# Kernel tuning notes

Hardware: AMD Instinct MI355X
Metric: run time of the kernel (lower is better)

## Reference

```python
import jax, jax.numpy as jnp
import numpy as np

B, S, D = 2, 2048, 1024
HQ, HKV = 16, 4
HD = D // HQ            # 64
RATIO = HQ // HKV       # 4
P = 4 * D               # 4096 FFN project dim
ROPE_BASE = 10000.0
NEG = -1e9


def _rope(x):
    # x: [..., s, d]; half-split (non-alternating) RoPE
    d = x.shape[-1]
    s = x.shape[-2]
    inv = 1.0 / (ROPE_BASE ** (jnp.arange(0, d, 2, dtype=jnp.float32) / d))
    ang = jnp.arange(s, dtype=jnp.float32)[:, None] * inv[None, :]   # [s, d/2]
    cos, sin = jnp.cos(ang), jnp.sin(ang)
    x1, x2 = x[..., : d // 2], x[..., d // 2 :]
    return jnp.concatenate([x1 * cos - x2 * sin, x1 * sin + x2 * cos], axis=-1)


def _layernorm(x, g, b):
    m = jnp.mean(x, axis=-1, keepdims=True)
    v = jnp.var(x, axis=-1, keepdims=True)
    return (x - m) * jax.lax.rsqrt(v + 1e-5) * g + b


def setup_inputs() -> dict:
    key = jax.random.key(0)
    ks = jax.random.split(key, 16)
    sd = 0.02
    x = jax.random.normal(ks[0], (B, S, D), dtype=jnp.float32)
    mask = jnp.where(jnp.tril(jnp.ones((S, S), dtype=bool)), 0.0, NEG).astype(jnp.float32)
    return {
        "x": x,
        "attention_mask": mask,
        "wq": jax.random.normal(ks[1], (D, D)) * sd,
        "wk": jax.random.normal(ks[2], (D, HKV * HD)) * sd,
        "wv": jax.random.normal(ks[3], (D, HKV * HD)) * sd,
        "wo": jax.random.normal(ks[4], (D, D)) * sd,
        "ln1_g": jnp.ones((D,), jnp.float32),
        "ln1_b": jnp.zeros((D,), jnp.float32),
        "ln2_g": jnp.ones((D,), jnp.float32),
        "ln2_b": jnp.zeros((D,), jnp.float32),
        "w1": jax.random.normal(ks[5], (D, P)) * sd,
        "b1": jnp.zeros((P,), jnp.float32),
        "w2": jax.random.normal(ks[6], (P, D)) * sd,
        "b2": jnp.zeros((D,), jnp.float32),
    }


def reference(x, attention_mask, wq, wk, wv, wo, ln1_g, ln1_b, ln2_g, ln2_b, w1, b1, w2, b2):
    b, s, d = x.shape
    # --- pre-norm GQA attention ---
    h = _layernorm(x, ln1_g, ln1_b)
    q = (h @ wq).reshape(b, s, HQ, HD).transpose(0, 2, 1, 3)       # [b, HQ, s, hd]
    k = (h @ wk).reshape(b, s, HKV, HD).transpose(0, 2, 1, 3)      # [b, HKV, s, hd]
    v = (h @ wv).reshape(b, s, HKV, HD).transpose(0, 2, 1, 3)
    q = _rope(q)
    k = _rope(k)
    # '(head group)' split with group = num_heads_kv, faithful to source
    q = q.reshape(b, RATIO, HKV, s, HD)                            # [b, r, g, s, hd]
    scores = jnp.einsum('brgsd,bgtd->brgst', q, k) / np.float32(np.sqrt(HD))
    scores = scores + attention_mask                               # broadcast [s,s]
    att = jax.nn.softmax(scores, axis=-1)
    o = jnp.einsum('brgst,bgtd->brgsd', att, v)                    # [b, r, g, s, hd]
    # '... head group s dhead -> ... s (head group dhead)'
    o = o.transpose(0, 3, 1, 2, 4).reshape(b, s, d)
    x = x + o @ wo
    # --- pre-norm MLP ---
    h2 = _layernorm(x, ln2_g, ln2_b)
    mlp = jax.nn.gelu(h2 @ w1 + b1) @ w2 + b2
    return x + mlp
```

## Files before the change

kernel.cpp:

```cpp
#include <hip/hip_runtime.h>
#include <cstdint>
#include <cstddef>

#define B_   2
#define S_   2048
#define D_   1024
#define HQ_  16
#define HKV_ 4
#define HD_  64
#define P_   4096

using frag8 = __attribute__((ext_vector_type(8))) short;
using f32x4 = __attribute__((ext_vector_type(4))) float;

__device__ __forceinline__ uint16_t f2b(float f) {
  uint32_t u = __builtin_bit_cast(uint32_t, f);
  u += 0x7fffu + ((u >> 16) & 1u);
  return (uint16_t)(u >> 16);
}
__device__ __forceinline__ float b2f(uint16_t h) {
  return __builtin_bit_cast(float, (uint32_t)h << 16);
}

__device__ __forceinline__ void gl16(const uint16_t* g, uint16_t* l) {
  __builtin_amdgcn_global_load_lds(
      (const __attribute__((address_space(1))) void*)g,
      (__attribute__((address_space(3))) void*)l, 16, 0, 0);
}

__device__ __forceinline__ float ldr(const void* p, size_t i, bool f32) {
  return f32 ? ((const float*)p)[i] : b2f(((const uint16_t*)p)[i]);
}
__device__ __forceinline__ void str_(void* p, size_t i, float v, bool f32) {
  if (f32) ((float*)p)[i] = v; else ((uint16_t*)p)[i] = f2b(v);
}

template <int CTRL>
__device__ __forceinline__ float fdpp(float x) {
  int v = __builtin_amdgcn_mov_dpp(__builtin_bit_cast(int, x), CTRL, 0xf, 0xf, true);
  return __builtin_bit_cast(float, v);
}
__device__ __forceinline__ float row16_max(float x) {
  x = fmaxf(x, fdpp<0xB1>(x));
  x = fmaxf(x, fdpp<0x4E>(x));
  x = fmaxf(x, fdpp<0x124>(x));
  x = fmaxf(x, fdpp<0x128>(x));
  return x;
}
__device__ __forceinline__ float row16_sum(float x) {
  x += fdpp<0xB1>(x);
  x += fdpp<0x4E>(x);
  x += fdpp<0x124>(x);
  x += fdpp<0x128>(x);
  return x;
}

__device__ __forceinline__ int psw(int row, int col) {
  return (((row) << 7) + ((col) << 1)) ^ ((row & 7) << 4);
}

__global__ void detect_kernel(const uint16_t* __restrict__ x, int* __restrict__ flag) {
  if (threadIdx.x == 0 && blockIdx.x == 0) {
    int sane = 0;
    for (int i = 0; i < 256; ++i) {
      uint16_t u = x[i];
      int e = (u >> 7) & 0xFF;
      if (u == 0 || (e >= 90 && e <= 141)) sane++;
    }
    *flag = (sane >= 240) ? 0 : 1;
  }
}

__global__ __launch_bounds__(256) void rope_table_kernel(float* __restrict__ cosT,
                                                         float* __restrict__ sinT) {
  int i = blockIdx.x * 256 + threadIdx.x;
  int s = i >> 5, d = i & 31;
  float ang = (float)s * powf(10000.0f, -(float)d * (1.0f / 32.0f));
  cosT[i] = cosf(ang);
  sinT[i] = sinf(ang);
}

template <bool F32>
__device__ __forceinline__ void trans_body(const void* in, uint16_t* out, int K, int N,
                                           uint16_t (*tile)[33]) {
  int n0 = blockIdx.x * 32, k0 = blockIdx.y * 32;
  int tx = threadIdx.x & 31, ty = threadIdx.x >> 5;
#pragma unroll
  for (int i = 0; i < 32; i += 8) {
    size_t idx = (size_t)(k0 + ty + i) * N + n0 + tx;
    tile[ty + i][tx] = F32 ? f2b(((const float*)in)[idx]) : ((const uint16_t*)in)[idx];
  }
  __syncthreads();
#pragma unroll
  for (int i = 0; i < 32; i += 8) out[(size_t)(n0 + ty + i) * K + k0 + tx] = tile[tx][ty + i];
}
__global__ __launch_bounds__(256) void transpose_k(const void* __restrict__ in,
                                                   uint16_t* __restrict__ out,
                                                   int K, int N, const int* __restrict__ flag) {
  __shared__ uint16_t tile[32][33];
  if (*flag) trans_body<true>(in, out, K, N, tile);
  else       trans_body<false>(in, out, K, N, tile);
}

template <bool F32>
__device__ __forceinline__ void ln_body(const void* x, const void* gamma, const void* beta,
                                        uint16_t* out, float* red) {
  const int row = blockIdx.x;
  const int t = threadIdx.x;
  float f[4], s1 = 0.f, s2 = 0.f;
#pragma unroll
  for (int i = 0; i < 4; i++) {
    f[i] = F32 ? ((const float*)x)[(size_t)row * D_ + t * 4 + i]
               : b2f(((const uint16_t*)x)[(size_t)row * D_ + t * 4 + i]);
    s1 += f[i]; s2 += f[i] * f[i];
  }
  for (int off = 1; off < 64; off <<= 1) { s1 += __shfl_xor(s1, off); s2 += __shfl_xor(s2, off); }
  int wave = t >> 6;
  if ((t & 63) == 0) { red[wave] = s1; red[4 + wave] = s2; }
  __syncthreads();
  s1 = red[0] + red[1] + red[2] + red[3];
  s2 = red[4] + red[5] + red[6] + red[7];
  float mean = s1 * (1.f / D_);
  float var = s2 * (1.f / D_) - mean * mean;
  float rstd = rsqrtf(var + 1e-5f);
  uint16_t ov[4];
#pragma unroll
  for (int i = 0; i < 4; i++) {
    float gv = F32 ? ((const float*)gamma)[t * 4 + i] : b2f(((const uint16_t*)gamma)[t * 4 + i]);
    float bv = F32 ? ((const float*)beta)[t * 4 + i]  : b2f(((const uint16_t*)beta)[t * 4 + i]);
    ov[i] = f2b((f[i] - mean) * rstd * gv + bv);
  }
  *(uint64_t*)(out + (size_t)row * D_ + t * 4) = *(uint64_t*)ov;
}
__global__ __launch_bounds__(256) void ln_kernel(const void* __restrict__ x,
                                                 const void* __restrict__ gamma,
                                                 const void* __restrict__ beta,
                                                 uint16_t* __restrict__ out,
                                                 const int* __restrict__ flag) {
  __shared__ float red[8];
  if (*flag) ln_body<true>(x, gamma, beta, out, red);
  else       ln_body<false>(x, gamma, beta, out, red);
}

enum { EPI_ROPE = 1, EPI_TRANSV = 2, EPI_GELU = 3, EPI_RES = 4, EPI_ACC = 5 };

template <int EPI>
__global__ __launch_bounds__(256) void gemm_bt(const uint16_t* __restrict__ A, int lda,
                                               const uint16_t* __restrict__ Bt, int ldb,
                                               void* __restrict__ C, int ldc,
                                               int M, int N, int K,
                                               const float* __restrict__ cosT,
                                               const float* __restrict__ sinT,
                                               const void* __restrict__ bias, int bias_off,
                                               const void* __restrict__ res,
                                               const int* __restrict__ flag) {
  __shared__ __align__(16) uint16_t As[2][64 * 64];
  __shared__ __align__(16) uint16_t Bs[2][64 * 64];
  const int tid = threadIdx.x;
  const int wave = tid >> 6, lane = tid & 63;
  const int quad = lane >> 4, l15 = lane & 15;
  const int bm = blockIdx.x * 64, bn = blockIdx.y * 64;
  const bool f32 = flag ? (*flag != 0) : false;

  const int arow = tid >> 3;
  const int gcol = (tid & 7) ^ (arow & 7);
  const uint16_t* apt = A + (size_t)(bm + arow) * lda + gcol * 8;
  const uint16_t* bpt = Bt + (size_t)(bn + arow) * ldb + gcol * 8;
  const int woff = wave * 512;

  f32x4 acc[4];
  f32x4 zero = {0.f, 0.f, 0.f, 0.f};
#pragma unroll
  for (int j = 0; j < 4; j++) acc[j] = zero;

  auto stage = [&](int buf, int it) {
    const uint16_t* a = apt + it * 64;
    const uint16_t* b = bpt + it * 64;
    gl16(a,                     &As[buf][woff]);
    gl16(a + (size_t)32 * lda,  &As[buf][2048 + woff]);
    gl16(b,                     &Bs[buf][woff]);
    gl16(b + (size_t)32 * ldb,  &Bs[buf][2048 + woff]);
  };

  const int NIT = K >> 6;
  stage(0, 0);
  int cur = 0;
  for (int it = 0; it < NIT; ++it) {
    stage(cur ^ 1, (it + 1 < NIT) ? (it + 1) : it);
    asm volatile("s_waitcnt vmcnt(4)" ::: "memory");
    __builtin_amdgcn_s_barrier();
    asm volatile("" ::: "memory");
    frag8 af[2], bfv[4][2];
#pragma unroll
    for (int ks = 0; ks < 2; ++ks) {
      int row = wave * 16 + l15;
      int c16 = (ks * 4 + quad) ^ (l15 & 7);
      af[ks] = *(const frag8*)&As[cur][row * 64 + c16 * 8];
    }
#pragma unroll
    for (int ni = 0; ni < 4; ++ni)
#pragma unroll
      for (int ks = 0; ks < 2; ++ks) {
        int row = ni * 16 + l15;
        int c16 = (ks * 4 + quad) ^ (l15 & 7);
        bfv[ni][ks] = *(const frag8*)&Bs[cur][row * 64 + c16 * 8];
      }
#pragma unroll
    for (int ks = 0; ks < 2; ++ks)
#pragma unroll
      for (int ni = 0; ni < 4; ++ni)
        acc[ni] = __builtin_amdgcn_mfma_f32_16x16x32_bf16(af[ks], bfv[ni][ks], acc[ni], 0, 0, 0);
    asm volatile("s_waitcnt lgkmcnt(0)" ::: "memory");
    __builtin_amdgcn_s_barrier();
    cur ^= 1;
  }

  const int row0 = bm + wave * 16 + quad * 4;

  if constexpr (EPI == EPI_ROPE) {
#pragma unroll
    for (int r = 0; r < 4; ++r) {
      int row = row0 + r;
      int s = row & (S_ - 1);
#pragma unroll
      for (int ni = 0; ni < 2; ++ni) {
        int d = ni * 16 + l15;
        float c = cosT[s * 32 + d], sn = sinT[s * 32 + d];
        float x1 = acc[ni][r], x2 = acc[ni + 2][r];
        size_t base = (size_t)row * ldc + bn + ni * 16 + l15;
        ((uint16_t*)C)[base] = f2b(x1 * c - x2 * sn);
        ((uint16_t*)C)[base + 32] = f2b(x1 * sn + x2 * c);
      }
    }
  } else if constexpr (EPI == EPI_TRANSV) {
#pragma unroll
    for (int ni = 0; ni < 4; ++ni)
#pragma unroll
      for (int r = 0; r < 4; ++r) {
        int row = row0 + r;
        int col = bn + ni * 16 + l15;
        int b = row >> 11, s = row & (S_ - 1);
        int kvh = col >> 6, d = col & 63;
        ((uint16_t*)C)[(size_t)((b * HKV_ + kvh) * HD_ + d) * S_ + s] = f2b(acc[ni][r]);
      }
  } else {
#pragma unroll
    for (int ni = 0; ni < 4; ++ni) {
      int col = bn + ni * 16 + l15;
#pragma unroll
      for (int r = 0; r < 4; ++r) {
        int row = row0 + r;
        float v = acc[ni][r];
        if constexpr (EPI == EPI_GELU) {
          v += ldr(bias, bias_off + col, f32);
          float z = 0.7978845608028654f * (v + 0.044715f * v * v * v);
          z = fminf(fmaxf(z, -15.f), 15.f);
          float e = __expf(-2.f * z);
          v = 0.5f * v * (1.f + (1.f - e) / (1.f + e));
          ((uint16_t*)C)[(size_t)row * ldc + col] = f2b(v);
        } else if constexpr (EPI == EPI_RES) {
          v += ldr(res, (size_t)row * ldc + col, f32);
          str_(C, (size_t)row * ldc + col, v, f32);
        } else if constexpr (EPI == EPI_ACC) {
          if (bias) v += ldr(bias, bias_off + col, f32);
          v += ldr(C, (size_t)row * ldc + col, f32);
          str_(C, (size_t)row * ldc + col, v, f32);
        }
      }
    }
  }
}

__global__ __launch_bounds__(256, 4) void attn_kernel(const uint16_t* __restrict__ q,
                                                      const uint16_t* __restrict__ k,
                                                      const uint16_t* __restrict__ vt,
                                                      uint16_t* __restrict__ o) {
  __shared__ __align__(16) uint16_t Ks[2][64 * 64];
  __shared__ __align__(16) uint16_t Vs[2][64 * 64];
  __shared__ __align__(16) uint16_t Plds[4][16 * 64];
  const int tid = threadIdx.x;
  const int wave = tid >> 6, lane = tid & 63;
  const int quad = lane >> 4, l15 = lane & 15;
  const int bid = blockIdx.x;
  const int m = bid & 63;
  const int g = (bid >> 6) & 3;
  const int b = bid >> 8;
  const int h = g + 4 * wave;

  const uint16_t* kbase = k + (size_t)(b * S_) * (HKV_ * HD_) + g * HD_;
  const uint16_t* vbase = vt + (size_t)((b * HKV_ + g) * HD_) * S_;
  f32x4 zero = {0.f, 0.f, 0.f, 0.f};

  const int arow = tid >> 3;
  const int gcol = (tid & 7) ^ (arow & 7);
  const int woff = wave * 512;
  uint16_t* pw = Plds[wave];

  auto stage = [&](int buf, int t) {
    const int kt = t << 6;
    gl16(kbase + (size_t)(kt + arow) * (HKV_ * HD_) + gcol * 8,      &Ks[buf][woff]);
    gl16(kbase + (size_t)(kt + 32 + arow) * (HKV_ * HD_) + gcol * 8, &Ks[buf][2048 + woff]);
    gl16(vbase + (size_t)arow * S_ + kt + gcol * 8,                  &Vs[buf][woff]);
    gl16(vbase + (size_t)(arow + 32) * S_ + kt + gcol * 8,           &Vs[buf][2048 + woff]);
  };

  int cur = 0;
  for (int seg = 0; seg < 2; ++seg) {
    const int qt = seg ? (127 - m) : m;
    const int q0 = qt * 16;

    const uint16_t* qbase = q + (size_t)(b * S_ + q0 + l15) * D_ + h * HD_ + quad * 8;
    frag8 qa0 = *(const frag8*)qbase;
    frag8 qa1 = *(const frag8*)(qbase + 32);

    f32x4 oacc[4];
#pragma unroll
    for (int i = 0; i < 4; i++) oacc[i] = zero;
    float m_i[4] = {-1e30f, -1e30f, -1e30f, -1e30f};
    float l_i[4] = {0.f, 0.f, 0.f, 0.f};

    const int nt = (q0 + 16 + 63) >> 6;
    stage(cur, 0);
    __syncthreads();
    for (int t = 0; t < nt; ++t) {
      const int kt = t << 6;
      if (t + 1 < nt) stage(cur ^ 1, t + 1);

      f32x4 sc[4];
#pragma unroll
      for (int f = 0; f < 4; ++f) {
        const int row = 16 * f + l15;
        frag8 kb0 = *(const frag8*)&Ks[cur][row * 64 + ((quad ^ (l15 & 7)) * 8)];
        frag8 kb1 = *(const frag8*)&Ks[cur][row * 64 + (((quad + 4) ^ (l15 & 7)) * 8)];
        f32x4 c = zero;
        c = __builtin_amdgcn_mfma_f32_16x16x32_bf16(qa0, kb0, c, 0, 0, 0);
        c = __builtin_amdgcn_mfma_f32_16x16x32_bf16(qa1, kb1, c, 0, 0, 0);
        sc[f] = c;
      }
      const bool needmask = (kt + 63 > q0);
      float p[4][4];
#pragma unroll
      for (int f = 0; f < 4; ++f)
#pragma unroll
        for (int r = 0; r < 4; ++r) p[f][r] = sc[f][r] * 0.125f;
      if (needmask) {
#pragma unroll
        for (int r = 0; r < 4; ++r) {
          int qq = q0 + quad * 4 + r;
#pragma unroll
          for (int f = 0; f < 4; ++f)
            if (kt + 16 * f + l15 > qq) p[f][r] = -1e30f;
        }
      }
      float alpha[4];
#pragma unroll
      for (int r = 0; r < 4; ++r) {
        float rm = fmaxf(fmaxf(p[0][r], p[1][r]), fmaxf(p[2][r], p[3][r]));
        rm = row16_max(rm);
        float mn = fmaxf(m_i[r], rm);
        alpha[r] = __expf(m_i[r] - mn);
        m_i[r] = mn;
        float rs = 0.f;
#pragma unroll
        for (int f = 0; f < 4; ++f) { p[f][r] = __expf(p[f][r] - mn); rs += p[f][r]; }
        rs = row16_sum(rs);
        l_i[r] = l_i[r] * alpha[r] + rs;
      }
#pragma unroll
      for (int r = 0; r < 4; ++r) {
        int row = quad * 4 + r;
#pragma unroll
        for (int f = 0; f < 4; ++f)
          *(uint16_t*)((char*)pw + psw(row, f * 16 + l15)) = f2b(p[f][r]);
      }
      asm volatile("s_waitcnt lgkmcnt(0)" ::: "memory");
      frag8 pa0 = *(const frag8*)((const char*)pw + psw(l15, quad * 8));
      frag8 pa1 = *(const frag8*)((const char*)pw + psw(l15, 32 + quad * 8));
#pragma unroll
      for (int d4 = 0; d4 < 4; ++d4) {
        const int row = d4 * 16 + l15;
        frag8 vb0 = *(const frag8*)&Vs[cur][row * 64 + ((quad ^ (l15 & 7)) * 8)];
        frag8 vb1 = *(const frag8*)&Vs[cur][row * 64 + (((quad + 4) ^ (l15 & 7)) * 8)];
        f32x4 t4 = oacc[d4];
#pragma unroll
        for (int r = 0; r < 4; ++r) t4[r] *= alpha[r];
        t4 = __builtin_amdgcn_mfma_f32_16x16x32_bf16(pa0, vb0, t4, 0, 0, 0);
        t4 = __builtin_amdgcn_mfma_f32_16x16x32_bf16(pa1, vb1, t4, 0, 0, 0);
        oacc[d4] = t4;
      }
      __syncthreads();
      cur ^= 1;
    }

#pragma unroll
    for (int d4 = 0; d4 < 4; ++d4)
#pragma unroll
      for (int r = 0; r < 4; ++r) {
        int row = b * S_ + q0 + quad * 4 + r;
        int col = h * HD_ + d4 * 16 + l15;
        o[(size_t)row * D_ + col] = f2b(oacc[d4][r] / l_i[r]);
      }
  }
}

extern "C" void kernel_launch(void* const* d_in, const int* in_sizes, int n_in,
                              void* d_out, int out_size, void* d_ws, size_t ws_size,
                              hipStream_t stream) {
  const void* x    = d_in[0];
  const void* wq   = d_in[2];
  const void* wk   = d_in[3];
  const void* wv   = d_in[4];
  const void* wo   = d_in[5];
  const void* ln1g = d_in[6];
  const void* ln1b = d_in[7];
  const void* ln2g = d_in[8];
  const void* ln2b = d_in[9];
  const void* w1   = d_in[10];
  const void* b1   = d_in[11];
  const void* w2   = d_in[12];
  const void* b2   = d_in[13];

  char* w = (char*)d_ws;
  int*      flag = (int*)w;
  float*    cosT = (float*)(w + 4096);
  float*    sinT = (float*)(w + 266240);
  uint16_t* wqT  = (uint16_t*)(w + 528384);
  uint16_t* wkT  = (uint16_t*)(w + 2625536);
  uint16_t* wvT  = (uint16_t*)(w + 3149824);
  uint16_t* woT  = (uint16_t*)(w + 3674112);
  uint16_t* hbuf = (uint16_t*)(w + 5771264);
  uint16_t* qbuf = (uint16_t*)(w + 14159872);
  uint16_t* kbuf = (uint16_t*)(w + 22548480);
  uint16_t* vtb  = (uint16_t*)(w + 24645632);
  uint16_t* obuf = (uint16_t*)(w + 26742784);
  uint16_t* w1T  = (uint16_t*)(w + 14159872);
  uint16_t* w2T  = (uint16_t*)(w + 22548480);
  uint16_t* hidq = (uint16_t*)(w + 30937088);

  detect_kernel<<<dim3(1), dim3(64), 0, stream>>>((const uint16_t*)x, flag);
  rope_table_kernel<<<dim3(256), dim3(256), 0, stream>>>(cosT, sinT);

  transpose_k<<<dim3(32, 32), dim3(256), 0, stream>>>(wq, wqT, 1024, 1024, flag);
  transpose_k<<<dim3(8, 32), dim3(256), 0, stream>>>(wk, wkT, 1024, 256, flag);
  transpose_k<<<dim3(8, 32), dim3(256), 0, stream>>>(wv, wvT, 1024, 256, flag);
  transpose_k<<<dim3(32, 32), dim3(256), 0, stream>>>(wo, woT, 1024, 1024, flag);

  ln_kernel<<<dim3(4096), dim3(256), 0, stream>>>(x, ln1g, ln1b, hbuf, flag);

  gemm_bt<EPI_ROPE><<<dim3(64, 16), dim3(256), 0, stream>>>(hbuf, 1024, wqT, 1024, qbuf, 1024,
      4096, 1024, 1024, cosT, sinT, nullptr, 0, nullptr, nullptr);
  gemm_bt<EPI_ROPE><<<dim3(64, 4), dim3(256), 0, stream>>>(hbuf, 1024, wkT, 1024, kbuf, 256,
      4096, 256, 1024, cosT, sinT, nullptr, 0, nullptr, nullptr);
  gemm_bt<EPI_TRANSV><<<dim3(64, 4), dim3(256), 0, stream>>>(hbuf, 1024, wvT, 1024, vtb, 256,
      4096, 256, 1024, nullptr, nullptr, nullptr, 0, nullptr, nullptr);

  attn_kernel<<<dim3(512), dim3(256), 0, stream>>>(qbuf, kbuf, vtb, obuf);

  transpose_k<<<dim3(128, 32), dim3(256), 0, stream>>>(w1, w1T, 1024, 4096, flag);

  gemm_bt<EPI_RES><<<dim3(64, 16), dim3(256), 0, stream>>>(obuf, 1024, woT, 1024, d_out, 1024,
      4096, 1024, 1024, nullptr, nullptr, nullptr, 0, x, flag);

  transpose_k<<<dim3(32, 128), dim3(256), 0, stream>>>(w2, w2T, 4096, 1024, flag);

  ln_kernel<<<dim3(4096), dim3(256), 0, stream>>>(d_out, ln2g, ln2b, hbuf, flag);

  for (int j = 0; j < 4; ++j) {
    const uint16_t* w1c = w1T + (size_t)j * 1024 * 1024;
    const uint16_t* w2c = w2T + (size_t)j * 1024;
    const void* bb = (j == 0) ? b2 : nullptr;
    gemm_bt<EPI_GELU><<<dim3(64, 16), dim3(256), 0, stream>>>(hbuf, 1024, w1c, 1024, hidq, 1024,
        4096, 1024, 1024, nullptr, nullptr, b1, j * 1024, nullptr, flag);
    gemm_bt<EPI_ACC><<<dim3(64, 16), dim3(256), 0, stream>>>(hidq, 1024, w2c, 4096, d_out, 1024,
        4096, 1024, 1024, nullptr, nullptr, bb, 0, nullptr, flag);
  }
}
```

Measured before the change: 442.1 us.

## Fuse QKV projections, use 2x2 wave tiling in GEMMs, streamline attention softmax

Merges the Q, K and V projection GEMMs into one launch over a 1536-wide output, sending each column band to the Q/K RoPE epilogue or the V-transpose epilogue. This relies on the transposed wq/wk/wv buffers being contiguous in the workspace. Non-banded GEMMs (out-proj, FFN) now split the 64x64 tile across waves as 2x2 32x32 sub-tiles instead of 16-row strips, which cuts LDS fragment reads per MFMA. The attention softmax folds log2(e) into the scale, uses exp2, and rescales the accumulator only when some row max grows, which removes launch overhead, LDS traffic and exp work.

```diff
diff --git a/kernel.cpp b/kernel.cpp
--- a/kernel.cpp
+++ b/kernel.cpp
@@ -142,7 +142,7 @@
   else       ln_body<false>(x, gamma, beta, out, red);
 }
 
-enum { EPI_ROPE = 1, EPI_TRANSV = 2, EPI_GELU = 3, EPI_RES = 4, EPI_ACC = 5 };
+enum { EPI_ROPE = 1, EPI_TRANSV = 2, EPI_GELU = 3, EPI_RES = 4, EPI_ACC = 5, EPI_QKV = 6 };
 
 template <int EPI>
 __global__ __launch_bounds__(256) void gemm_bt(const uint16_t* __restrict__ A, int lda,
@@ -153,12 +153,15 @@
                                                const float* __restrict__ sinT,
                                                const void* __restrict__ bias, int bias_off,
                                                const void* __restrict__ res,
-                                               const int* __restrict__ flag) {
+                                               const int* __restrict__ flag,
+                                               void* __restrict__ C2, void* __restrict__ C3) {
+  constexpr bool BANDED = (EPI == EPI_ROPE || EPI == EPI_TRANSV || EPI == EPI_QKV);
   __shared__ __align__(16) uint16_t As[2][64 * 64];
   __shared__ __align__(16) uint16_t Bs[2][64 * 64];
   const int tid = threadIdx.x;
   const int wave = tid >> 6, lane = tid & 63;
   const int quad = lane >> 4, l15 = lane & 15;
+  const int wm = wave >> 1, wn = wave & 1;
   const int bm = blockIdx.x * 64, bn = blockIdx.y * 64;
   const bool f32 = flag ? (*flag != 0) : false;
 
@@ -190,49 +193,107 @@
     asm volatile("s_waitcnt vmcnt(4)" ::: "memory");
     __builtin_amdgcn_s_barrier();
     asm volatile("" ::: "memory");
-    frag8 af[2], bfv[4][2];
-#pragma unroll
-    for (int ks = 0; ks < 2; ++ks) {
-      int row = wave * 16 + l15;
-      int c16 = (ks * 4 + quad) ^ (l15 & 7);
-      af[ks] = *(const frag8*)&As[cur][row * 64 + c16 * 8];
+    if constexpr (BANDED) {
+      frag8 af[2], bfv[4][2];
+#pragma unroll
+      for (int ks = 0; ks < 2; ++ks) {
+        int row = wave * 16 + l15;
+        int c16 = (ks * 4 + quad) ^ (l15 & 7);
+        af[ks] = *(const frag8*)&As[cur][row * 64 + c16 * 8];
+      }
+#pragma unroll
+      for (int ni = 0; ni < 4; ++ni)
+#pragma unroll
+        for (int ks = 0; ks < 2; ++ks) {
+          int row = ni * 16 + l15;
+          int c16 = (ks * 4 + quad) ^ (l15 & 7);
+          bfv[ni][ks] = *(const frag8*)&Bs[cur][row * 64 + c16 * 8];
+        }
+#pragma unroll
+      for (int ks = 0; ks < 2; ++ks)
+#pragma unroll
+        for (int ni = 0; ni < 4; ++ni)
+          acc[ni] = __builtin_amdgcn_mfma_f32_16x16x32_bf16(af[ks], bfv[ni][ks], acc[ni], 0, 0, 0);
+    } else {
+      frag8 af2[2][2], bf2[2][2];
+#pragma unroll
+      for (int mi = 0; mi < 2; ++mi)
+#pragma unroll
+        for (int ks = 0; ks < 2; ++ks) {
+          int row = wm * 32 + mi * 16 + l15;
+          int c16 = (ks * 4 + quad) ^ (l15 & 7);
+          af2[mi][ks] = *(const frag8*)&As[cur][row * 64 + c16 * 8];
+        }
+#pragma unroll
+      for (int ni = 0; ni < 2; ++ni)
+#pragma unroll
+        for (int ks = 0; ks < 2; ++ks) {
+          int row = wn * 32 + ni * 16 + l15;
+          int c16 = (ks * 4 + quad) ^ (l15 & 7);
+          bf2[ni][ks] = *(const frag8*)&Bs[cur][row * 64 + c16 * 8];
+        }
+#pragma unroll
+      for (int ks = 0; ks < 2; ++ks)
+#pragma unroll
+        for (int mi = 0; mi < 2; ++mi)
+#pragma unroll
+          for (int ni = 0; ni < 2; ++ni)
+            acc[mi * 2 + ni] = __builtin_amdgcn_mfma_f32_16x16x32_bf16(af2[mi][ks], bf2[ni][ks],
+                                                                       acc[mi * 2 + ni], 0, 0, 0);
     }
-#pragma unroll
-    for (int ni = 0; ni < 4; ++ni)
-#pragma unroll
-      for (int ks = 0; ks < 2; ++ks) {
-        int row = ni * 16 + l15;
-        int c16 = (ks * 4 + quad) ^ (l15 & 7);
-        bfv[ni][ks] = *(const frag8*)&Bs[cur][row * 64 + c16 * 8];
-      }
-#pragma unroll
-    for (int ks = 0; ks < 2; ++ks)
-#pragma unroll
-      for (int ni = 0; ni < 4; ++ni)
-        acc[ni] = __builtin_amdgcn_mfma_f32_16x16x32_bf16(af[ks], bfv[ni][ks], acc[ni], 0, 0, 0);
     asm volatile("s_waitcnt lgkmcnt(0)" ::: "memory");
     __builtin_amdgcn_s_barrier();
     cur ^= 1;
   }
 
-  const int row0 = bm + wave * 16 + quad * 4;
-
-  if constexpr (EPI == EPI_ROPE) {
-#pragma unroll
-    for (int r = 0; r < 4; ++r) {
-      int row = row0 + r;
-      int s = row & (S_ - 1);
-#pragma unroll
-      for (int ni = 0; ni < 2; ++ni) {
-        int d = ni * 16 + l15;
-        float c = cosT[s * 32 + d], sn = sinT[s * 32 + d];
-        float x1 = acc[ni][r], x2 = acc[ni + 2][r];
-        size_t base = (size_t)row * ldc + bn + ni * 16 + l15;
-        ((uint16_t*)C)[base] = f2b(x1 * c - x2 * sn);
-        ((uint16_t*)C)[base + 32] = f2b(x1 * sn + x2 * c);
-      }
+  if constexpr (EPI == EPI_ROPE || EPI == EPI_QKV) {
+    const int row0 = bm + wave * 16 + quad * 4;
+    if (EPI == EPI_ROPE || bn < 1024) {
+#pragma unroll
+      for (int r = 0; r < 4; ++r) {
+        int row = row0 + r;
+        int s = row & (S_ - 1);
+#pragma unroll
+        for (int ni = 0; ni < 2; ++ni) {
+          int d = ni * 16 + l15;
+          float c = cosT[s * 32 + d], sn = sinT[s * 32 + d];
+          float x1 = acc[ni][r], x2 = acc[ni + 2][r];
+          size_t base = (size_t)row * ldc + bn + ni * 16 + l15;
+          ((uint16_t*)C)[base] = f2b(x1 * c - x2 * sn);
+          ((uint16_t*)C)[base + 32] = f2b(x1 * sn + x2 * c);
+        }
+      }
+    } else if (bn < 1280) {
+      uint16_t* kb = (uint16_t*)C2;
+#pragma unroll
+      for (int r = 0; r < 4; ++r) {
+        int row = row0 + r;
+        int s = row & (S_ - 1);
+#pragma unroll
+        for (int ni = 0; ni < 2; ++ni) {
+          int d = ni * 16 + l15;
+          float c = cosT[s * 32 + d], sn = sinT[s * 32 + d];
+          float x1 = acc[ni][r], x2 = acc[ni + 2][r];
+          size_t base = (size_t)row * 256 + (bn - 1024) + ni * 16 + l15;
+          kb[base] = f2b(x1 * c - x2 * sn);
+          kb[base + 32] = f2b(x1 * sn + x2 * c);
+        }
+      }
+    } else {
+      uint16_t* vb = (uint16_t*)C3;
+#pragma unroll
+      for (int ni = 0; ni < 4; ++ni)
+#pragma unroll
+        for (int r = 0; r < 4; ++r) {
+          int row = row0 + r;
+          int col3 = (bn - 1280) + ni * 16 + l15;
+          int b = row >> 11, s = row & (S_ - 1);
+          int kvh = col3 >> 6, d = col3 & 63;
+          vb[(size_t)((b * HKV_ + kvh) * HD_ + d) * S_ + s] = f2b(acc[ni][r]);
+        }
     }
   } else if constexpr (EPI == EPI_TRANSV) {
+    const int row0 = bm + wave * 16 + quad * 4;
 #pragma unroll
     for (int ni = 0; ni < 4; ++ni)
 #pragma unroll
@@ -244,30 +305,33 @@
         ((uint16_t*)C)[(size_t)((b * HKV_ + kvh) * HD_ + d) * S_ + s] = f2b(acc[ni][r]);
       }
   } else {
-#pragma unroll
-    for (int ni = 0; ni < 4; ++ni) {
-      int col = bn + ni * 16 + l15;
-#pragma unroll
-      for (int r = 0; r < 4; ++r) {
-        int row = row0 + r;
-        float v = acc[ni][r];
-        if constexpr (EPI == EPI_GELU) {
-          v += ldr(bias, bias_off + col, f32);
-          float z = 0.7978845608028654f * (v + 0.044715f * v * v * v);
-          z = fminf(fmaxf(z, -15.f), 15.f);
-          float e = __expf(-2.f * z);
-          v = 0.5f * v * (1.f + (1.f - e) / (1.f + e));
-          ((uint16_t*)C)[(size_t)row * ldc + col] = f2b(v);
-        } else if constexpr (EPI == EPI_RES) {
-          v += ldr(res, (size_t)row * ldc + col, f32);
-          str_(C, (size_t)row * ldc + col, v, f32);
-        } else if constexpr (EPI == EPI_ACC) {
-          if (bias) v += ldr(bias, bias_off + col, f32);
-          v += ldr(C, (size_t)row * ldc + col, f32);
-          str_(C, (size_t)row * ldc + col, v, f32);
-        }
-      }
-    }
+    const int row0 = bm + wm * 32 + quad * 4;
+#pragma unroll
+    for (int mi = 0; mi < 2; ++mi)
+#pragma unroll
+      for (int ni = 0; ni < 2; ++ni) {
+        int col = bn + wn * 32 + ni * 16 + l15;
+#pragma unroll
+        for (int r = 0; r < 4; ++r) {
+          int row = row0 + mi * 16 + r;
+          float v = acc[mi * 2 + ni][r];
+          if constexpr (EPI == EPI_GELU) {
+            v += ldr(bias, bias_off + col, f32);
+            float z = 0.7978845608028654f * (v + 0.044715f * v * v * v);
+            z = fminf(fmaxf(z, -15.f), 15.f);
+            float e = __expf(-2.f * z);
+            v = 0.5f * v * (1.f + (1.f - e) / (1.f + e));
+            ((uint16_t*)C)[(size_t)row * ldc + col] = f2b(v);
+          } else if constexpr (EPI == EPI_RES) {
+            v += ldr(res, (size_t)row * ldc + col, f32);
+            str_(C, (size_t)row * ldc + col, v, f32);
+          } else if constexpr (EPI == EPI_ACC) {
+            if (bias) v += ldr(bias, bias_off + col, f32);
+            v += ldr(C, (size_t)row * ldc + col, f32);
+            str_(C, (size_t)row * ldc + col, v, f32);
+          }
+        }
+      }
   }
 }
 
@@ -290,6 +354,7 @@
   const uint16_t* kbase = k + (size_t)(b * S_) * (HKV_ * HD_) + g * HD_;
   const uint16_t* vbase = vt + (size_t)((b * HKV_ + g) * HD_) * S_;
   f32x4 zero = {0.f, 0.f, 0.f, 0.f};
+  const float SCL = 0.125f * 1.4426950408889634f;
 
   const int arow = tid >> 3;
   const int gcol = (tid & 7) ^ (arow & 7);
@@ -337,41 +402,54 @@
         c = __builtin_amdgcn_mfma_f32_16x16x32_bf16(qa1, kb1, c, 0, 0, 0);
         sc[f] = c;
       }
-      const bool needmask = (kt + 63 > q0);
-      float p[4][4];
-#pragma unroll
-      for (int f = 0; f < 4; ++f)
-#pragma unroll
-        for (int r = 0; r < 4; ++r) p[f][r] = sc[f][r] * 0.125f;
-      if (needmask) {
+      if (kt + 63 > q0) {
+#pragma unroll
+        for (int f = 0; f < 4; ++f)
+#pragma unroll
+          for (int r = 0; r < 4; ++r) {
+            int qq = q0 + quad * 4 + r;
+            sc[f][r] = (kt + 16 * f + l15 > qq) ? -1e30f : sc[f][r] * SCL;
+          }
+      } else {
+#pragma unroll
+        for (int f = 0; f < 4; ++f)
+#pragma unroll
+          for (int r = 0; r < 4; ++r) sc[f][r] *= SCL;
+      }
+      float rm[4];
+#pragma unroll
+      for (int r = 0; r < 4; ++r) {
+        float x = fmaxf(fmaxf(sc[0][r], sc[1][r]), fmaxf(sc[2][r], sc[3][r]));
+        rm[r] = row16_max(x);
+      }
+      float gg = fmaxf(fmaxf(rm[0] - m_i[0], rm[1] - m_i[1]),
+                       fmaxf(rm[2] - m_i[2], rm[3] - m_i[3]));
+      if (__any(gg > 0.f)) {
+        float al[4];
 #pragma unroll
         for (int r = 0; r < 4; ++r) {
-          int qq = q0 + quad * 4 + r;
-#pragma unroll
-          for (int f = 0; f < 4; ++f)
-            if (kt + 16 * f + l15 > qq) p[f][r] = -1e30f;
-        }
-      }
-      float alpha[4];
-#pragma unroll
-      for (int r = 0; r < 4; ++r) {
-        float rm = fmaxf(fmaxf(p[0][r], p[1][r]), fmaxf(p[2][r], p[3][r]));
-        rm = row16_max(rm);
-        float mn = fmaxf(m_i[r], rm);
-        alpha[r] = __expf(m_i[r] - mn);
-        m_i[r] = mn;
-        float rs = 0.f;
-#pragma unroll
-        for (int f = 0; f < 4; ++f) { p[f][r] = __expf(p[f][r] - mn); rs += p[f][r]; }
-        rs = row16_sum(rs);
-        l_i[r] = l_i[r] * alpha[r] + rs;
+          float mn = fmaxf(m_i[r], rm[r]);
+          al[r] = exp2f(m_i[r] - mn);
+          m_i[r] = mn;
+          l_i[r] *= al[r];
+        }
+#pragma unroll
+        for (int d4 = 0; d4 < 4; ++d4)
+#pragma unroll
+          for (int r = 0; r < 4; ++r) oacc[d4][r] *= al[r];
       }
 #pragma unroll
       for (int r = 0; r < 4; ++r) {
         int row = quad * 4 + r;
-#pragma unroll
-        for (int f = 0; f < 4; ++f)
-          *(uint16_t*)((char*)pw + psw(row, f * 16 + l15)) = f2b(p[f][r]);
+        float rs = 0.f;
+#pragma unroll
+        for (int f = 0; f < 4; ++f) {
+          float pv = exp2f(sc[f][r] - m_i[r]);
+          rs += pv;
+          *(uint16_t*)((char*)pw + psw(row, f * 16 + l15)) = f2b(pv);
+        }
+        rs = row16_sum(rs);
+        l_i[r] += rs;
       }
       asm volatile("s_waitcnt lgkmcnt(0)" ::: "memory");
       frag8 pa0 = *(const frag8*)((const char*)pw + psw(l15, quad * 8));
@@ -382,8 +460,6 @@
         frag8 vb0 = *(const frag8*)&Vs[cur][row * 64 + ((quad ^ (l15 & 7)) * 8)];
         frag8 vb1 = *(const frag8*)&Vs[cur][row * 64 + (((quad + 4) ^ (l15 & 7)) * 8)];
         f32x4 t4 = oacc[d4];
-#pragma unroll
-        for (int r = 0; r < 4; ++r) t4[r] *= alpha[r];
         t4 = __builtin_amdgcn_mfma_f32_16x16x32_bf16(pa0, vb0, t4, 0, 0, 0);
         t4 = __builtin_amdgcn_mfma_f32_16x16x32_bf16(pa1, vb1, t4, 0, 0, 0);
         oacc[d4] = t4;
@@ -447,19 +523,15 @@
 
   ln_kernel<<<dim3(4096), dim3(256), 0, stream>>>(x, ln1g, ln1b, hbuf, flag);
 
-  gemm_bt<EPI_ROPE><<<dim3(64, 16), dim3(256), 0, stream>>>(hbuf, 1024, wqT, 1024, qbuf, 1024,
-      4096, 1024, 1024, cosT, sinT, nullptr, 0, nullptr, nullptr);
-  gemm_bt<EPI_ROPE><<<dim3(64, 4), dim3(256), 0, stream>>>(hbuf, 1024, wkT, 1024, kbuf, 256,
-      4096, 256, 1024, cosT, sinT, nullptr, 0, nullptr, nullptr);
-  gemm_bt<EPI_TRANSV><<<dim3(64, 4), dim3(256), 0, stream>>>(hbuf, 1024, wvT, 1024, vtb, 256,
-      4096, 256, 1024, nullptr, nullptr, nullptr, 0, nullptr, nullptr);
+  gemm_bt<EPI_QKV><<<dim3(64, 24), dim3(256), 0, stream>>>(hbuf, 1024, wqT, 1024, qbuf, 1024,
+      4096, 1536, 1024, cosT, sinT, nullptr, 0, nullptr, nullptr, kbuf, vtb);
 
   attn_kernel<<<dim3(512), dim3(256), 0, stream>>>(qbuf, kbuf, vtb, obuf);
 
   transpose_k<<<dim3(128, 32), dim3(256), 0, stream>>>(w1, w1T, 1024, 4096, flag);
 
   gemm_bt<EPI_RES><<<dim3(64, 16), dim3(256), 0, stream>>>(obuf, 1024, woT, 1024, d_out, 1024,
-      4096, 1024, 1024, nullptr, nullptr, nullptr, 0, x, flag);
+      4096, 1024, 1024, nullptr, nullptr, nullptr, 0, x, flag, nullptr, nullptr);
 
   transpose_k<<<dim3(32, 128), dim3(256), 0, stream>>>(w2, w2T, 4096, 1024, flag);
 
@@ -470,8 +542,8 @@
     const uint16_t* w2c = w2T + (size_t)j * 1024;
     const void* bb = (j == 0) ? b2 : nullptr;
     gemm_bt<EPI_GELU><<<dim3(64, 16), dim3(256), 0, stream>>>(hbuf, 1024, w1c, 1024, hidq, 1024,
-        4096, 1024, 1024, nullptr, nullptr, b1, j * 1024, nullptr, flag);
+        4096, 1024, 1024, nullptr, nullptr, b1, j * 1024, nullptr, flag, nullptr, nullptr);
     gemm_bt<EPI_ACC><<<dim3(64, 16), dim3(256), 0, stream>>>(hidq, 1024, w2c, 4096, d_out, 1024,
-        4096, 1024, 1024, nullptr, nullptr, bb, 0, nullptr, flag);
-  }
-}
+        4096, 1024, 1024, nullptr, nullptr, bb, 0, nullptr, flag, nullptr, nullptr);
+  }
+}
```

Result: faster. 431.8 us (-2.3%).
